# Optimization experiments

Measured on AMD Instinct MI355X. Metric: run time of the kernel, lower is better.

Reference implementation:

```python
import jax, jax.numpy as jnp
import numpy as np


def _gru_cell(x, h, W_ih, b_ih, W_hh, b_hh):
    # torch.nn.GRUCell math, gate order (r, z, n)
    gi = x @ W_ih.T + b_ih
    gh = h @ W_hh.T + b_hh
    ir, iz, inn = jnp.split(gi, 3, axis=-1)
    hr, hz, hn = jnp.split(gh, 3, axis=-1)
    r = jax.nn.sigmoid(ir + hr)
    zg = jax.nn.sigmoid(iz + hz)
    n = jnp.tanh(inn + r * hn)
    return (1.0 - zg) * n + zg * h


def setup_inputs() -> dict:
    key = jax.random.key(0)
    ks = jax.random.split(key, 16)
    B, T = 16384, 24
    MLP, Z, H = 1024, 32, 128
    NS, NP = 6, 2               # n_state, n_pred_state
    IN = MLP + Z + 2 * NP       # GRUCell input size = 1060
    f = lambda k, s, sc=1.0: jax.random.normal(k, s, dtype=jnp.float32) * sc
    return {
        "last_obs_state": f(ks[0], (B, NS)),
        "enc_h_feat": f(ks[1], (B, MLP)),
        "z": f(ks[2], (B, Z)),
        "sg": f(ks[3], (B, NP)),
        "fut_traj": f(ks[4], (T, B, NS)),
        # dec_hidden: Linear(mlp_dim+z_dim -> dec_h_dim)
        "W_dh": f(ks[5], (H, MLP + Z), 0.03),
        "b_dh": jnp.zeros((H,), jnp.float32),
        # to_vel: Linear(6 -> 2)
        "W_vel": f(ks[6], (NP, NS), 0.3),
        "b_vel": jnp.zeros((NP,), jnp.float32),
        # GRUCell weights
        "W_ih": f(ks[7], (3 * H, IN), 0.03),
        "b_ih": jnp.zeros((3 * H,), jnp.float32),
        "W_hh": f(ks[8], (3 * H, H), 0.08),
        "b_hh": jnp.zeros((3 * H,), jnp.float32),
        # fc_mu, fc_std: Linear(dec_h_dim -> 2)
        "W_mu": f(ks[9], (NP, H), 0.08),
        "b_mu": jnp.zeros((NP,), jnp.float32),
        "W_std": f(ks[10], (NP, H), 0.08),
        "b_std": jnp.zeros((NP,), jnp.float32),
    }


def reference(last_obs_state, enc_h_feat, z, sg, fut_traj,
              W_dh, b_dh, W_vel, b_vel, W_ih, b_ih, W_hh, b_hh,
              W_mu, b_mu, W_std, b_std):
    dt = 0.4 * 12
    zx = jnp.concatenate([enc_h_feat, z], axis=1)          # (B, mlp+z)
    h0 = zx @ W_dh.T + b_dh                                 # (B, H)
    a0 = last_obs_state @ W_vel.T + b_vel                   # (B, 2)
    rel = (sg - last_obs_state[:, :2]) / dt                 # (B, 2)
    # teacher forcing: a at step i is a0 for i=0, else fut_traj[i-1,:,2:4]
    a_seq = jnp.concatenate([a0[None], fut_traj[:-1, :, 2:4]], axis=0)  # (T,B,2)

    def step(h, a):
        x = jnp.concatenate([zx, a, rel], axis=1)           # (B, mlp+z+4)
        h = _gru_cell(x, h, W_ih, b_ih, W_hh, b_hh)
        mu = h @ W_mu.T + b_mu
        std = jnp.sqrt(jnp.exp(h @ W_std.T + b_std))
        return h, (mu, std)

    _, (mus, stds) = jax.lax.scan(step, h0, a_seq)
    return mus, stds  # each (T, B, 2): parameters of the returned Normal
```

## Files before the change

### kernel.cpp

```cpp
#include <hip/hip_runtime.h>

typedef __attribute__((ext_vector_type(4))) short short4v;
typedef __attribute__((ext_vector_type(8))) short short8;
typedef __attribute__((ext_vector_type(4))) float floatx4;

#define NB 16384
#define TT 24
#define HH 128
#define LDA 40
#define LDH 168
#define ASZ (32 * LDA)
#define HSZ (32 * LDH)
#define MUS_OFF 0
#define STD_OFF (TT * NB * 2)

__device__ __forceinline__ float bf2f(unsigned short u) {
    union { unsigned int i; float f; } v; v.i = ((unsigned int)u) << 16; return v.f;
}
__device__ __forceinline__ unsigned short f2bf(float f) {
    union { float f; unsigned int i; } v; v.f = f;
    unsigned int x = v.i;
    return (unsigned short)((x + 0x7fffu + ((x >> 16) & 1u)) >> 16);
}
__device__ __forceinline__ float fsig(float x) {
    return __fdividef(1.f, 1.f + __expf(-x));
}
__device__ __forceinline__ float ftanh(float x) {
    x = fminf(15.f, fmaxf(-15.f, x));
    float e = __expf(2.f * x);
    return __fdividef(e - 1.f, e + 1.f);
}
__device__ __forceinline__ short4v pk4(floatx4 a) {
    short4v r;
    r[0] = (short)f2bf(a[0]); r[1] = (short)f2bf(a[1]);
    r[2] = (short)f2bf(a[2]); r[3] = (short)f2bf(a[3]);
    return r;
}
__device__ __forceinline__ unsigned int pk2(float a, float b) {
    return (unsigned int)f2bf(a) | ((unsigned int)f2bf(b) << 16);
}
__device__ __forceinline__ float upk(unsigned int u, int hi) {
    union { unsigned int i; float f; } v;
    v.i = hi ? (u & 0xffff0000u) : (u << 16);
    return v.f;
}

__global__ void k_prep(const float* __restrict__ W_ih, const float* __restrict__ W_dh,
                       const float* __restrict__ W_hh, const float* __restrict__ b_hh,
                       const float* __restrict__ W_mu, const float* __restrict__ W_std,
                       unsigned short* __restrict__ Wc, unsigned short* __restrict__ Whh,
                       unsigned short* __restrict__ Wms) {
    int blk = blockIdx.x, t = threadIdx.x;
    if (blk < 512) {
        const float* src = (blk < 384) ? (W_ih + (size_t)blk * 1060)
                                       : (W_dh + (size_t)(blk - 384) * 1056);
        unsigned short* dst = Wc + (size_t)blk * 1056;
        for (int k = t; k < 1056; k += 256) dst[k] = f2bf(src[k]);
    } else if (blk < 896) {
        int r = blk - 512;
        int g = r >> 7;
        unsigned short* dst = Whh + (size_t)r * 160;
        if (t < 128) dst[t] = f2bf(W_hh[(size_t)r * 128 + t]);
        else if (t == 128) dst[128] = (g < 2) ? f2bf(W_ih[(size_t)r * 1060 + 1056]) : 0;
        else if (t == 129) dst[129] = (g < 2) ? f2bf(W_ih[(size_t)r * 1060 + 1057]) : 0;
        else if (t == 130) dst[130] = (g == 2) ? f2bf(b_hh[r]) : 0;
        else if (t < 160) dst[t] = 0;
    } else {
        for (int i = t; i < 512; i += 256) {
            int r = i >> 7, k = i & 127;
            Wms[i] = f2bf(r < 2 ? W_mu[r * 128 + k] : W_std[(r - 2) * 128 + k]);
        }
    }
}

__global__ __launch_bounds__(512, 4) void k_fused(
    const float* __restrict__ last, const float* __restrict__ enc,
    const float* __restrict__ zin, const float* __restrict__ sg,
    const float* __restrict__ fut, const float* __restrict__ b_dh,
    const float* __restrict__ W_vel, const float* __restrict__ b_vel,
    const float* __restrict__ W_ih, const float* __restrict__ b_ih,
    const float* __restrict__ b_hh, const float* __restrict__ b_mu,
    const float* __restrict__ b_std, const unsigned short* __restrict__ Wc,
    const unsigned short* __restrict__ Whh, const unsigned short* __restrict__ Wms,
    float* __restrict__ out) {
    __shared__ unsigned short As[2 * ASZ];
    __shared__ unsigned short h2[2 * HSZ];
    __shared__ unsigned short wms_lds[512];
    __shared__ float rel_lds[32][2];

    const int tid = threadIdx.x;
    const int w = tid >> 6, lane = tid & 63;
    const int col = lane & 15, q = lane >> 4;
    const int b0 = blockIdx.x * 32;
    const int jc = w * 16 + col;

    const int etask = tid >> 2, epart = tid & 3;
    const int erow = etask >> 2, ekind = (etask >> 1) & 1, ec = etask & 1;
    const float ebias = ekind ? b_std[ec] : b_mu[ec];

    if (tid < 512) wms_lds[tid] = Wms[tid];
    for (int i = tid; i < 2 * 32 * 32; i += 512) {
        int buf = i >> 10, loc = i & 1023, row = loc >> 5, kk = loc & 31;
        if (buf == 0 && kk < 2) continue;
        h2[buf * HSZ + row * LDH + 128 + kk] = (kk == 2) ? (unsigned short)0x3F80 : 0;
    }
    if (tid < 64) {
        int row = tid >> 1, c = tid & 1, b = b0 + row;
        float s = b_vel[c];
#pragma unroll
        for (int s2 = 0; s2 < 6; s2++) s += last[b * 6 + s2] * W_vel[c * 6 + s2];
        h2[row * LDH + 128 + c] = f2bf(s);
        rel_lds[row][c] = (sg[b * 2 + c] - last[b * 6 + c]) * (1.f / 4.8f);
    }

    floatx4 acc2[2][4];
#pragma unroll
    for (int i = 0; i < 2; i++)
#pragma unroll
        for (int j = 0; j < 4; j++) acc2[i][j] = (floatx4){0.f, 0.f, 0.f, 0.f};

    const int arow = tid >> 3, koff = (tid & 7) * 4;
    if (tid < 256) {
        floatx4 a0 = *(const floatx4*)(enc + (size_t)(b0 + arow) * 1024 + koff);
        *(short4v*)(As + arow * LDA + koff) = pk4(a0);
    }
    __syncthreads();

    for (int ki = 0; ki < 33; ki++) {
        const int cur = ki & 1;
        floatx4 an;
        if (tid < 256 && ki < 32) {
            an = (ki + 1 < 32)
                ? *(const floatx4*)(enc + (size_t)(b0 + arow) * 1024 + (ki + 1) * 32 + koff)
                : *(const floatx4*)(zin + (size_t)(b0 + arow) * 32 + koff);
        }
        short8 bb[4];
#pragma unroll
        for (int gg = 0; gg < 4; gg++)
            bb[gg] = *(const short8*)(Wc + (size_t)(gg * 128 + jc) * 1056 + ki * 32 + q * 8);
        short8 af[2];
#pragma unroll
        for (int mt = 0; mt < 2; mt++)
            af[mt] = *(const short8*)(As + cur * ASZ + (mt * 16 + col) * LDA + q * 8);
#pragma unroll
        for (int gg = 0; gg < 4; gg++)
#pragma unroll
            for (int mt = 0; mt < 2; mt++)
                acc2[mt][gg] = __builtin_amdgcn_mfma_f32_16x16x32_bf16(
                    af[mt], bb[gg], acc2[mt][gg], 0, 0, 0);
        if (tid < 256 && ki < 32) *(short4v*)(As + (cur ^ 1) * ASZ + arow * LDA + koff) = pk4(an);
        __syncthreads();
    }

    unsigned int gp[2][3][2];
    float hprev[2][4];
    {
        float bihg[3], wr0g[3], wr1g[3];
#pragma unroll
        for (int g = 0; g < 3; g++) {
            const size_t rb = (size_t)(g * HH + jc) * 1060;
            bihg[g] = b_ih[g * HH + jc] + ((g < 2) ? b_hh[g * HH + jc] : 0.f);
            wr0g[g] = W_ih[rb + 1058];
            wr1g[g] = W_ih[rb + 1059];
        }
        const float bdh = b_dh[jc];
#pragma unroll
        for (int mt = 0; mt < 2; mt++) {
            float gv[3][4];
#pragma unroll
            for (int r = 0; r < 4; r++) {
                int row = mt * 16 + q * 4 + r;
                float r0 = rel_lds[row][0], r1 = rel_lds[row][1];
#pragma unroll
                for (int g = 0; g < 3; g++)
                    gv[g][r] = acc2[mt][g][r] + bihg[g] + r0 * wr0g[g] + r1 * wr1g[g];
                float h0v = acc2[mt][3][r] + bdh;
                hprev[mt][r] = h0v;
                h2[row * LDH + jc] = f2bf(h0v);
            }
#pragma unroll
            for (int g = 0; g < 3; g++) {
                gp[mt][g][0] = pk2(gv[g][0], gv[g][1]);
                gp[mt][g][1] = pk2(gv[g][2], gv[g][3]);
            }
        }
    }

    short8 bfr[3][4];
#pragma unroll
    for (int g = 0; g < 3; g++)
#pragma unroll
        for (int kt = 0; kt < 4; kt++)
            bfr[g][kt] = *(const short8*)(Whh + (size_t)(g * HH + jc) * 160 + kt * 32 + q * 8);
    const float wan0 = W_ih[(size_t)(2 * HH + jc) * 1060 + 1056];
    const float wan1 = W_ih[(size_t)(2 * HH + jc) * 1060 + 1057];

    __syncthreads();

    for (int t = 0; t < TT; t++) {
        const unsigned short* hc = h2 + (t & 1) * HSZ;
        unsigned short* hn = h2 + ((t + 1) & 1) * HSZ;

        if (t > 0) {
            const unsigned short* hp = hc + erow * LDH + epart * 32;
            const unsigned short* wp = wms_lds + (ekind * 2 + ec) * 128 + epart * 32;
            float s = 0.f;
#pragma unroll
            for (int j = 0; j < 4; j++) {
                short8 hv = *(const short8*)(hp + j * 8);
                short8 wv = *(const short8*)(wp + j * 8);
#pragma unroll
                for (int e = 0; e < 8; e++)
                    s += bf2f((unsigned short)hv[e]) * bf2f((unsigned short)wv[e]);
            }
            s += __shfl_xor(s, 1);
            s += __shfl_xor(s, 2);
            if (epart == 0) {
                float val = s + ebias;
                if (ekind) val = __expf(0.5f * val);
                out[(ekind ? STD_OFF : MUS_OFF) + ((size_t)(t - 1) * NB + b0 + erow) * 2 + ec] = val;
            }
        }

        floatx4 acc[2][3];
#pragma unroll
        for (int mt = 0; mt < 2; mt++)
#pragma unroll
            for (int g = 0; g < 3; g++) acc[mt][g] = (floatx4){0.f, 0.f, 0.f, 0.f};
#pragma unroll
        for (int kt = 0; kt < 4; kt++) {
            short8 af2[2];
#pragma unroll
            for (int mt = 0; mt < 2; mt++)
                af2[mt] = *(const short8*)(hc + (mt * 16 + col) * LDH + kt * 32 + q * 8);
#pragma unroll
            for (int mt = 0; mt < 2; mt++)
#pragma unroll
                for (int g = 0; g < 3; g++)
                    acc[mt][g] = __builtin_amdgcn_mfma_f32_16x16x32_bf16(
                        af2[mt], bfr[g][kt], acc[mt][g], 0, 0, 0);
        }
        {
            short8 af4[2], k4f[3];
#pragma unroll
            for (int g = 0; g < 3; g++)
                k4f[g] = *(const short8*)(Whh + (size_t)(g * HH + jc) * 160 + 128 + q * 8);
#pragma unroll
            for (int mt = 0; mt < 2; mt++)
                af4[mt] = *(const short8*)(hc + (mt * 16 + col) * LDH + 128 + q * 8);
#pragma unroll
            for (int mt = 0; mt < 2; mt++)
#pragma unroll
                for (int g = 0; g < 3; g++)
                    acc[mt][g] = __builtin_amdgcn_mfma_f32_16x16x32_bf16(
                        af4[mt], k4f[g], acc[mt][g], 0, 0, 0);
        }

#pragma unroll
        for (int mt = 0; mt < 2; mt++) {
#pragma unroll
            for (int r = 0; r < 4; r++) {
                int row = mt * 16 + q * 4 + r;
                unsigned int ap = *(const unsigned int*)(hc + row * LDH + 128);
                float a0v = upk(ap, 0), a1v = upk(ap, 1);
                float gir = upk(gp[mt][0][r >> 1], r & 1) + acc[mt][0][r];
                float giz = upk(gp[mt][1][r >> 1], r & 1) + acc[mt][1][r];
                float gin = upk(gp[mt][2][r >> 1], r & 1) + a0v * wan0 + a1v * wan1;
                float ghn = acc[mt][2][r];
                float rg = fsig(gir);
                float zg = fsig(giz);
                float ng = ftanh(gin + rg * ghn);
                hprev[mt][r] = (1.f - zg) * ng + zg * hprev[mt][r];
                hn[row * LDH + jc] = f2bf(hprev[mt][r]);
            }
        }
        if (tid >= 448) {
            int i = tid - 448, row = i >> 1, c = i & 1;
            hn[row * LDH + 128 + c] = f2bf(fut[((size_t)t * NB + b0 + row) * 6 + 2 + c]);
        }
        __syncthreads();
    }

    {
        const unsigned short* hc = h2;
        const unsigned short* hp = hc + erow * LDH + epart * 32;
        const unsigned short* wp = wms_lds + (ekind * 2 + ec) * 128 + epart * 32;
        float s = 0.f;
#pragma unroll
        for (int j = 0; j < 4; j++) {
            short8 hv = *(const short8*)(hp + j * 8);
            short8 wv = *(const short8*)(wp + j * 8);
#pragma unroll
            for (int e = 0; e < 8; e++)
                s += bf2f((unsigned short)hv[e]) * bf2f((unsigned short)wv[e]);
        }
        s += __shfl_xor(s, 1);
        s += __shfl_xor(s, 2);
        if (epart == 0) {
            float val = s + ebias;
            if (ekind) val = __expf(0.5f * val);
            out[(ekind ? STD_OFF : MUS_OFF) + ((size_t)(TT - 1) * NB + b0 + erow) * 2 + ec] = val;
        }
    }
}

extern "C" void kernel_launch(void* const* d_in, const int* in_sizes, int n_in,
                              void* d_out, int out_size, void* d_ws, size_t ws_size,
                              hipStream_t stream) {
    (void)in_sizes; (void)n_in; (void)out_size; (void)ws_size;
    const float* last  = (const float*)d_in[0];
    const float* enc   = (const float*)d_in[1];
    const float* zin   = (const float*)d_in[2];
    const float* sg    = (const float*)d_in[3];
    const float* fut   = (const float*)d_in[4];
    const float* b_dh  = (const float*)d_in[6];
    const float* W_vel = (const float*)d_in[7];
    const float* b_vel = (const float*)d_in[8];
    const float* W_ih  = (const float*)d_in[9];
    const float* b_ih  = (const float*)d_in[10];
    const float* W_hh  = (const float*)d_in[11];
    const float* b_hh  = (const float*)d_in[12];
    const float* W_mu  = (const float*)d_in[13];
    const float* b_mu  = (const float*)d_in[14];
    const float* W_std = (const float*)d_in[15];
    const float* b_std = (const float*)d_in[16];
    const float* W_dh  = (const float*)d_in[5];
    float* out = (float*)d_out;

    char* ws = (char*)d_ws;
    unsigned short* Wc  = (unsigned short*)ws;
    unsigned short* Whh = (unsigned short*)(ws + 1081344);
    unsigned short* Wms = (unsigned short*)(ws + 1204224);

    k_prep<<<897, 256, 0, stream>>>(W_ih, W_dh, W_hh, b_hh, W_mu, W_std, Wc, Whh, Wms);
    k_fused<<<512, 512, 0, stream>>>(last, enc, zin, sg, fut, b_dh, W_vel, b_vel,
                                     W_ih, b_ih, b_hh, b_mu, b_std, Wc, Whh, Wms, out);
}
```

Measured before the change: 339.2 us.

## Compute mu/std heads with MFMA in wave 0 and stream W_hh fragments per step

Replaces the scalar bf16 dot-product head (all threads, with shuffles) with MFMA accumulation on wave 0. It uses a padded 16x160 head weight matrix whose bias sits in column 130, which multiplies the constant-one column of the hidden buffer. The W_hh B-fragments are no longer held in registers across the loop and are reloaded from global/L2 each step, merging the extra k-tile into a 5-iteration loop. This frees registers and cuts ALU work, but adds repeated global weight loads and leaves extra head work on wave 0 only. It also simplifies the GRU blend to one FMA form.

```diff
diff --git a/kernel.cpp b/kernel.cpp
--- a/kernel.cpp
+++ b/kernel.cpp
@@ -47,9 +47,10 @@
 
 __global__ void k_prep(const float* __restrict__ W_ih, const float* __restrict__ W_dh,
                        const float* __restrict__ W_hh, const float* __restrict__ b_hh,
-                       const float* __restrict__ W_mu, const float* __restrict__ W_std,
+                       const float* __restrict__ W_mu, const float* __restrict__ b_mu,
+                       const float* __restrict__ W_std, const float* __restrict__ b_std,
                        unsigned short* __restrict__ Wc, unsigned short* __restrict__ Whh,
-                       unsigned short* __restrict__ Wms) {
+                       unsigned short* __restrict__ WmsE) {
     int blk = blockIdx.x, t = threadIdx.x;
     if (blk < 512) {
         const float* src = (blk < 384) ? (W_ih + (size_t)blk * 1060)
@@ -66,9 +67,14 @@
         else if (t == 130) dst[130] = (g == 2) ? f2bf(b_hh[r]) : 0;
         else if (t < 160) dst[t] = 0;
     } else {
-        for (int i = t; i < 512; i += 256) {
-            int r = i >> 7, k = i & 127;
-            Wms[i] = f2bf(r < 2 ? W_mu[r * 128 + k] : W_std[(r - 2) * 128 + k]);
+        for (int i = t; i < 16 * 160; i += 256) {
+            int r = i / 160, k = i - r * 160;
+            unsigned short v = 0;
+            if (r < 4) {
+                if (k < 128) v = f2bf(r < 2 ? W_mu[r * 128 + k] : W_std[(r - 2) * 128 + k]);
+                else if (k == 130) v = f2bf(r < 2 ? b_mu[r] : b_std[r - 2]);
+            }
+            WmsE[i] = v;
         }
     }
 }
@@ -79,13 +85,11 @@
     const float* __restrict__ fut, const float* __restrict__ b_dh,
     const float* __restrict__ W_vel, const float* __restrict__ b_vel,
     const float* __restrict__ W_ih, const float* __restrict__ b_ih,
-    const float* __restrict__ b_hh, const float* __restrict__ b_mu,
-    const float* __restrict__ b_std, const unsigned short* __restrict__ Wc,
-    const unsigned short* __restrict__ Whh, const unsigned short* __restrict__ Wms,
+    const float* __restrict__ b_hh, const unsigned short* __restrict__ Wc,
+    const unsigned short* __restrict__ Whh, const unsigned short* __restrict__ WmsE,
     float* __restrict__ out) {
     __shared__ unsigned short As[2 * ASZ];
     __shared__ unsigned short h2[2 * HSZ];
-    __shared__ unsigned short wms_lds[512];
     __shared__ float rel_lds[32][2];
 
     const int tid = threadIdx.x;
@@ -94,11 +98,6 @@
     const int b0 = blockIdx.x * 32;
     const int jc = w * 16 + col;
 
-    const int etask = tid >> 2, epart = tid & 3;
-    const int erow = etask >> 2, ekind = (etask >> 1) & 1, ec = etask & 1;
-    const float ebias = ekind ? b_std[ec] : b_mu[ec];
-
-    if (tid < 512) wms_lds[tid] = Wms[tid];
     for (int i = tid; i < 2 * 32 * 32; i += 512) {
         int buf = i >> 10, loc = i & 1023, row = loc >> 5, kk = loc & 31;
         if (buf == 0 && kk < 2) continue;
@@ -186,12 +185,6 @@
         }
     }
 
-    short8 bfr[3][4];
-#pragma unroll
-    for (int g = 0; g < 3; g++)
-#pragma unroll
-        for (int kt = 0; kt < 4; kt++)
-            bfr[g][kt] = *(const short8*)(Whh + (size_t)(g * HH + jc) * 160 + kt * 32 + q * 8);
     const float wan0 = W_ih[(size_t)(2 * HH + jc) * 1060 + 1056];
     const float wan1 = W_ih[(size_t)(2 * HH + jc) * 1060 + 1057];
 
@@ -201,34 +194,21 @@
         const unsigned short* hc = h2 + (t & 1) * HSZ;
         unsigned short* hn = h2 + ((t + 1) & 1) * HSZ;
 
-        if (t > 0) {
-            const unsigned short* hp = hc + erow * LDH + epart * 32;
-            const unsigned short* wp = wms_lds + (ekind * 2 + ec) * 128 + epart * 32;
-            float s = 0.f;
-#pragma unroll
-            for (int j = 0; j < 4; j++) {
-                short8 hv = *(const short8*)(hp + j * 8);
-                short8 wv = *(const short8*)(wp + j * 8);
-#pragma unroll
-                for (int e = 0; e < 8; e++)
-                    s += bf2f((unsigned short)hv[e]) * bf2f((unsigned short)wv[e]);
-            }
-            s += __shfl_xor(s, 1);
-            s += __shfl_xor(s, 2);
-            if (epart == 0) {
-                float val = s + ebias;
-                if (ekind) val = __expf(0.5f * val);
-                out[(ekind ? STD_OFF : MUS_OFF) + ((size_t)(t - 1) * NB + b0 + erow) * 2 + ec] = val;
-            }
-        }
-
         floatx4 acc[2][3];
+        floatx4 accms[2];
 #pragma unroll
         for (int mt = 0; mt < 2; mt++)
 #pragma unroll
             for (int g = 0; g < 3; g++) acc[mt][g] = (floatx4){0.f, 0.f, 0.f, 0.f};
-#pragma unroll
-        for (int kt = 0; kt < 4; kt++) {
+        accms[0] = (floatx4){0.f, 0.f, 0.f, 0.f};
+        accms[1] = (floatx4){0.f, 0.f, 0.f, 0.f};
+
+#pragma unroll
+        for (int kt = 0; kt < 5; kt++) {
+            short8 bfg[3];
+#pragma unroll
+            for (int g = 0; g < 3; g++)
+                bfg[g] = *(const short8*)(Whh + (size_t)(g * HH + jc) * 160 + kt * 32 + q * 8);
             short8 af2[2];
 #pragma unroll
             for (int mt = 0; mt < 2; mt++)
@@ -238,22 +218,27 @@
 #pragma unroll
                 for (int g = 0; g < 3; g++)
                     acc[mt][g] = __builtin_amdgcn_mfma_f32_16x16x32_bf16(
-                        af2[mt], bfr[g][kt], acc[mt][g], 0, 0, 0);
-        }
-        {
-            short8 af4[2], k4f[3];
-#pragma unroll
-            for (int g = 0; g < 3; g++)
-                k4f[g] = *(const short8*)(Whh + (size_t)(g * HH + jc) * 160 + 128 + q * 8);
-#pragma unroll
-            for (int mt = 0; mt < 2; mt++)
-                af4[mt] = *(const short8*)(hc + (mt * 16 + col) * LDH + 128 + q * 8);
-#pragma unroll
-            for (int mt = 0; mt < 2; mt++)
-#pragma unroll
-                for (int g = 0; g < 3; g++)
-                    acc[mt][g] = __builtin_amdgcn_mfma_f32_16x16x32_bf16(
-                        af4[mt], k4f[g], acc[mt][g], 0, 0, 0);
+                        af2[mt], bfg[g], acc[mt][g], 0, 0, 0);
+            if (w == 0 && t > 0) {
+                short8 msf = *(const short8*)(WmsE + (size_t)jc * 160 + kt * 32 + q * 8);
+#pragma unroll
+                for (int mt = 0; mt < 2; mt++)
+                    accms[mt] = __builtin_amdgcn_mfma_f32_16x16x32_bf16(
+                        af2[mt], msf, accms[mt], 0, 0, 0);
+            }
+        }
+
+        if (w == 0 && t > 0 && col < 4) {
+            int kind = col >> 1, c = col & 1;
+#pragma unroll
+            for (int mt = 0; mt < 2; mt++)
+#pragma unroll
+                for (int r = 0; r < 4; r++) {
+                    float val = accms[mt][r];
+                    if (kind) val = __expf(0.5f * val);
+                    int b = b0 + mt * 16 + q * 4 + r;
+                    out[(kind ? STD_OFF : MUS_OFF) + ((size_t)(t - 1) * NB + b) * 2 + c] = val;
+                }
         }
 
 #pragma unroll
@@ -270,7 +255,7 @@
                 float rg = fsig(gir);
                 float zg = fsig(giz);
                 float ng = ftanh(gin + rg * ghn);
-                hprev[mt][r] = (1.f - zg) * ng + zg * hprev[mt][r];
+                hprev[mt][r] = ng + zg * (hprev[mt][r] - ng);
                 hn[row * LDH + jc] = f2bf(hprev[mt][r]);
             }
         }
@@ -281,25 +266,32 @@
         __syncthreads();
     }
 
-    {
+    if (w == 0) {
         const unsigned short* hc = h2;
-        const unsigned short* hp = hc + erow * LDH + epart * 32;
-        const unsigned short* wp = wms_lds + (ekind * 2 + ec) * 128 + epart * 32;
-        float s = 0.f;
-#pragma unroll
-        for (int j = 0; j < 4; j++) {
-            short8 hv = *(const short8*)(hp + j * 8);
-            short8 wv = *(const short8*)(wp + j * 8);
-#pragma unroll
-            for (int e = 0; e < 8; e++)
-                s += bf2f((unsigned short)hv[e]) * bf2f((unsigned short)wv[e]);
-        }
-        s += __shfl_xor(s, 1);
-        s += __shfl_xor(s, 2);
-        if (epart == 0) {
-            float val = s + ebias;
-            if (ekind) val = __expf(0.5f * val);
-            out[(ekind ? STD_OFF : MUS_OFF) + ((size_t)(TT - 1) * NB + b0 + erow) * 2 + ec] = val;
+        floatx4 accms[2];
+        accms[0] = (floatx4){0.f, 0.f, 0.f, 0.f};
+        accms[1] = (floatx4){0.f, 0.f, 0.f, 0.f};
+#pragma unroll
+        for (int kt = 0; kt < 5; kt++) {
+            short8 msf = *(const short8*)(WmsE + (size_t)jc * 160 + kt * 32 + q * 8);
+#pragma unroll
+            for (int mt = 0; mt < 2; mt++) {
+                short8 af2 = *(const short8*)(hc + (mt * 16 + col) * LDH + kt * 32 + q * 8);
+                accms[mt] = __builtin_amdgcn_mfma_f32_16x16x32_bf16(
+                    af2, msf, accms[mt], 0, 0, 0);
+            }
+        }
+        if (col < 4) {
+            int kind = col >> 1, c = col & 1;
+#pragma unroll
+            for (int mt = 0; mt < 2; mt++)
+#pragma unroll
+                for (int r = 0; r < 4; r++) {
+                    float val = accms[mt][r];
+                    if (kind) val = __expf(0.5f * val);
+                    int b = b0 + mt * 16 + q * 4 + r;
+                    out[(kind ? STD_OFF : MUS_OFF) + ((size_t)(TT - 1) * NB + b) * 2 + c] = val;
+                }
         }
     }
 }
@@ -313,6 +305,7 @@
     const float* zin   = (const float*)d_in[2];
     const float* sg    = (const float*)d_in[3];
     const float* fut   = (const float*)d_in[4];
+    const float* W_dh  = (const float*)d_in[5];
     const float* b_dh  = (const float*)d_in[6];
     const float* W_vel = (const float*)d_in[7];
     const float* b_vel = (const float*)d_in[8];
@@ -324,15 +317,15 @@
     const float* b_mu  = (const float*)d_in[14];
     const float* W_std = (const float*)d_in[15];
     const float* b_std = (const float*)d_in[16];
-    const float* W_dh  = (const float*)d_in[5];
     float* out = (float*)d_out;
 
     char* ws = (char*)d_ws;
-    unsigned short* Wc  = (unsigned short*)ws;
-    unsigned short* Whh = (unsigned short*)(ws + 1081344);
-    unsigned short* Wms = (unsigned short*)(ws + 1204224);
-
-    k_prep<<<897, 256, 0, stream>>>(W_ih, W_dh, W_hh, b_hh, W_mu, W_std, Wc, Whh, Wms);
+    unsigned short* Wc   = (unsigned short*)ws;
+    unsigned short* Whh  = (unsigned short*)(ws + 1081344);
+    unsigned short* WmsE = (unsigned short*)(ws + 1204224);
+
+    k_prep<<<897, 256, 0, stream>>>(W_ih, W_dh, W_hh, b_hh, W_mu, b_mu, W_std, b_std,
+                                    Wc, Whh, WmsE);
     k_fused<<<512, 512, 0, stream>>>(last, enc, zin, sg, fut, b_dh, W_vel, b_vel,
-                                     W_ih, b_ih, b_hh, b_mu, b_std, Wc, Whh, Wms, out);
-}
+                                     W_ih, b_ih, b_hh, Wc, Whh, WmsE, out);
+}
```

New measurement: 394.4 us. 1.16x slower.
